# Kernel optimization log

Hardware: AMD Instinct MI355X
Metric: run time of the kernel (lower is better)

Reference implementation:

```python
import jax, jax.numpy as jnp
import numpy as np

D = 32        # dmodel (forced by reshape(..., 32) in the original)
N = 2000      # n_nodes == liner_fourth
SLOPE = 0.2   # LeakyReLU negative slope
EPS = 1e-6    # SublayerConnection LayerNorm eps (annotated-transformer style)


def _layernorm(x, g, b):
    m = x.mean(-1, keepdims=True)
    v = x.var(-1, keepdims=True)
    return g * (x - m) / jnp.sqrt(v + EPS) + b


def setup_inputs() -> dict:
    key = jax.random.key(0)
    ks = jax.random.split(key, 18)
    F_, NL, NS = 16, 500, 1500
    s = 0.1
    return {
        "state": jax.random.normal(ks[0], (F_, NS, D), jnp.float32),
        "left": jax.random.normal(ks[1], (F_, NL, D), jnp.float32),
        "inputad": jax.random.bernoulli(ks[2], 0.02, (F_, N, N)).astype(jnp.float32),
        "w3": s * jax.random.normal(ks[3], (D, D), jnp.float32),       # linearThird
        "b3": jnp.zeros((D,), jnp.float32),
        "attn_w": s * jax.random.normal(ks[4], (1, 2 * D), jnp.float32),  # attn (no bias)
        "w4": s * jax.random.normal(ks[5], (D, N), jnp.float32),       # linearFourth: 2000->32
        "b4": jnp.zeros((D,), jnp.float32),
        "w1": s * jax.random.normal(ks[6], (D, D), jnp.float32),       # linear
        "b1": jnp.zeros((D,), jnp.float32),
        "w_ih": s * jax.random.normal(ks[7], (4 * D, D), jnp.float32),  # LSTMCell (gate order i,f,g,o)
        "w_hh": s * jax.random.normal(ks[8], (4 * D, D), jnp.float32),
        "b_ih": jnp.zeros((4 * D,), jnp.float32),
        "b_hh": jnp.zeros((4 * D,), jnp.float32),
        "ln_g": jnp.ones((D,), jnp.float32),                            # SublayerConnection norm
        "ln_b": jnp.zeros((D,), jnp.float32),
        "w2": s * jax.random.normal(ks[9], (D, D), jnp.float32),        # linearSecond
        "b2": jnp.zeros((D,), jnp.float32),
    }


def reference(state, left, inputad, w3, b3, attn_w, w4, b4, w1, b1,
              w_ih, w_hh, b_ih, b_hh, ln_g, ln_b, w2, b2):
    # eval mode: all dropouts are identity
    x = jnp.concatenate([left, state], axis=1)          # [F, N, D]
    F_, n = x.shape[0], x.shape[1]
    g = x @ w3.T + b3                                   # [F, N, D]

    # torch: e = leaky(attn(cat([g.repeat_interleave(n,0), g.repeat(n,1,1)], -1)))
    # Decompose the linear over the concat: attn_w = [a_l | a_r].
    # g_repeat_interleave row m -> g[m // n]; g_repeat row m -> g[m % F_];
    # e.view(F_, n, n)[b, i, j] = e_flat[b*n + i, j].
    a_l, a_r = attn_w[0, :D], attn_w[0, D:]
    s_l = g @ a_l                                        # [F, N]
    s_r = g @ a_r                                        # [F, N]
    idx = (jnp.arange(F_)[:, None] * n + jnp.arange(n)[None, :]) % F_  # [F, N]
    e_mat = jax.nn.leaky_relu(s_l[:, None, :] + s_r[idx], SLOPE)       # [F, N, N]

    e_masked = jnp.where(inputad == 0, 0.0, e_mat)       # masked_fill(adj==0, 0)
    h = jax.nn.leaky_relu(jnp.einsum('bij,oj->bio', e_masked, w4) + b4, SLOPE)  # [F, N, 32]

    # first softmax(e)/dropout pair is dead code (overwritten); a = softmax(h, dim=1)
    a = jax.nn.softmax(h, axis=1)
    st = (a * g) @ w1.T + b1                             # elementwise branch (a.shape == g.shape)

    agg = jnp.matmul(inputad, st)                        # bmm(degree2, state): [F, N, D]

    # SublayerConnection: st + dropout(sublayer(norm(st))); sublayer = LSTMCell cell-state
    nx = _layernorm(st, ln_g, ln_b)
    c0 = nx.reshape(-1, D)                               # initial cell state = norm(st)
    # h0 = zeros, so the w_hh @ h0 contribution vanishes (b_hh still applies)
    gates = agg.reshape(-1, D) @ w_ih.T + b_ih + b_hh    # [F*N, 4D]
    i_g = jax.nn.sigmoid(gates[:, :D])
    f_g = jax.nn.sigmoid(gates[:, D:2 * D])
    g_g = jnp.tanh(gates[:, 2 * D:3 * D])
    c1 = f_g * c0 + i_g * g_g                            # LSTMCell returns (h', c'); [1] -> c'

    out = st + c1.reshape(F_, n, D)
    return out @ w2.T + b2
```

## Files before the change

### kernel.cpp

```cpp
#include <hip/hip_runtime.h>
#include <math.h>

#define F_    16
#define NROW  2000
#define NL    500
#define D     32
#define ROWS  (F_*NROW)
#define SLOPE 0.2f
#define CAP   128
#define LCAP  256

__global__ __launch_bounds__(256) void k1_g(
    const float* __restrict__ state, const float* __restrict__ left,
    const float* __restrict__ w3, const float* __restrict__ b3,
    const float* __restrict__ attn_w, const float* __restrict__ w4,
    float* __restrict__ g, float* __restrict__ s_l, float* __restrict__ s_r,
    float* __restrict__ w4t)
{
    int bid = blockIdx.x;
    int t = threadIdx.x;
    if (bid >= ROWS/8) {
        int k = (bid - ROWS/8) * 256 + t;
        if (k < D * NROW) {
            int o = k / NROW, j = k - o * NROW;
            w4t[j * D + o] = w4[k];
        }
        return;
    }
    __shared__ float sw3[D*33];
    __shared__ float sb3[D], sal[D], sar[D];
    for (int k = t; k < D*D; k += 256) sw3[(k>>5)*33 + (k&31)] = w3[k];
    if (t < D) { sb3[t] = b3[t]; sal[t] = attn_w[t]; sar[t] = attn_w[D + t]; }
    __syncthreads();
    int grp = t >> 5, lane = t & 31;
    int row = bid * 8 + grp;
    int b = row / NROW, i = row - b * NROW;
    const float* xrow = (i < NL) ? (left  + ((size_t)b * NL + i) * D)
                                 : (state + ((size_t)b * (NROW - NL) + (i - NL)) * D);
    float x = xrow[lane];
    float acc = sb3[lane];
#pragma unroll
    for (int k = 0; k < D; ++k)
        acc += __shfl(x, k, 32) * sw3[lane*33 + k];
    g[(size_t)row * D + lane] = acc;
    float pl = acc * sal[lane], pr = acc * sar[lane];
#pragma unroll
    for (int m = 16; m >= 1; m >>= 1) {
        pl += __shfl_xor(pl, m, 32);
        pr += __shfl_xor(pr, m, 32);
    }
    if (lane == 0) { s_l[row] = pl; s_r[row] = pr; }
}

__global__ __launch_bounds__(256) void k2_scan(
    const float* __restrict__ adj,
    const float* __restrict__ s_l, const float* __restrict__ s_r,
    const float* __restrict__ w4t, const float* __restrict__ b4,
    float* __restrict__ h, int* __restrict__ nzc, unsigned short* __restrict__ nzi)
{
    __shared__ int   sh_j[4][LCAP+1];
    __shared__ float sh_e[4][LCAP];
    int t = threadIdx.x;
    int w = t >> 6, lane = t & 63;
    int row = blockIdx.x * 4 + w;
    int b = row / NROW, i = row - b * NROW;
    int r = i & 15;
    const float4* mrow = reinterpret_cast<const float4*>(adj + (size_t)row * NROW);

    float4 v[8];
#pragma unroll
    for (int it = 0; it < 7; ++it)
        v[it] = mrow[it * 64 + lane];
    v[7] = make_float4(0.f, 0.f, 0.f, 0.f);
    if (448 + lane < NROW/4) v[7] = mrow[448 + lane];

    int c = 0;
#pragma unroll
    for (int it = 0; it < 8; ++it)
        c += (v[it].x != 0.f) + (v[it].y != 0.f) + (v[it].z != 0.f) + (v[it].w != 0.f);
    int inc = c;
#pragma unroll
    for (int off = 1; off < 64; off <<= 1) {
        int n = __shfl_up(inc, off, 64);
        inc += (lane >= off) ? n : 0;
    }
    int pos = inc - c;
    int cnt = __shfl(inc, 63, 64);

#pragma unroll
    for (int it = 0; it < 8; ++it) {
        int jb = (it * 64 + lane) * 4;
#pragma unroll
        for (int cc = 0; cc < 4; ++cc) {
            float val = (cc == 0) ? v[it].x : (cc == 1) ? v[it].y
                      : (cc == 2) ? v[it].z : v[it].w;
            int hit = (val != 0.f);
            int tgt = (hit && pos < LCAP) ? pos : LCAP;
            sh_j[w][tgt] = jb + cc;
            pos += hit;
        }
    }
    if (cnt > LCAP) cnt = LCAP;

    const float* slb = s_l + (size_t)b * NROW;
    const float* srr = s_r + (size_t)r * NROW;
    for (int k = lane; k < cnt; k += 64) {
        int j = sh_j[w][k];
        float e = slb[j] + srr[j];
        sh_e[w][k] = (e > 0.f) ? e : SLOPE * e;
    }

    int o = lane & 31, half = lane >> 5;
    float acc = 0.f;
    for (int k = half; k < cnt; k += 2)
        acc += sh_e[w][k] * w4t[sh_j[w][k] * D + o];
    acc += __shfl_xor(acc, 32, 64);
    if (lane < 32) {
        float hv = acc + b4[o];
        h[(size_t)row * D + o] = (hv > 0.f) ? hv : SLOPE * hv;
    }

    int cc2 = (cnt < CAP) ? cnt : CAP;
    for (int k = lane; k < cc2; k += 64)
        nzi[(size_t)row * CAP + k] = (unsigned short)sh_j[w][k];
    if (lane == 0) nzc[row] = cc2;
}

__global__ __launch_bounds__(256) void k3a_psum(const float* __restrict__ h,
                                                float* __restrict__ psum)
{
    int b = blockIdx.x, slice = blockIdx.y;
    int t = threadIdx.x;
    int o = t & 31, ti = t >> 5;
    int base = slice * 125;
    float s = 0.f;
    for (int i = base + ti; i < base + 125; i += 8)
        s += expf(h[((size_t)b * NROW + i) * D + o]);
    __shared__ float red[8][D];
    red[ti][o] = s;
    __syncthreads();
    if (t < D) {
        float tot = 0.f;
#pragma unroll
        for (int k = 0; k < 8; ++k) tot += red[k][t];
        psum[((size_t)b * 16 + slice) * D + t] = tot;
    }
}

__global__ __launch_bounds__(256) void k3b_st(
    const float* __restrict__ h, const float* __restrict__ g,
    const float* __restrict__ psum,
    const float* __restrict__ w1, const float* __restrict__ b1,
    float* __restrict__ st)
{
    __shared__ float sw1[D*33], sb1[D], ssum[D];
    int t = threadIdx.x;
    int bid = blockIdx.x;
    int b = bid / 250;
    for (int k = t; k < D*D; k += 256) sw1[(k>>5)*33 + (k&31)] = w1[k];
    if (t < D) {
        sb1[t] = b1[t];
        float tot = 0.f;
#pragma unroll
        for (int s = 0; s < 16; ++s) tot += psum[((size_t)b * 16 + s) * D + t];
        ssum[t] = tot;
    }
    __syncthreads();
    int grp = t >> 5, lane = t & 31;
    size_t row = (size_t)bid * 8 + grp;
    float p = (expf(h[row * D + lane]) / ssum[lane]) * g[row * D + lane];
    float acc = sb1[lane];
#pragma unroll
    for (int k = 0; k < D; ++k)
        acc += __shfl(p, k, 32) * sw1[lane*33 + k];
    st[row * D + lane] = acc;
}

__global__ __launch_bounds__(256) void k4_final(
    const float* __restrict__ st,
    const int* __restrict__ nzc, const unsigned short* __restrict__ nzi,
    const float* __restrict__ w_ih, const float* __restrict__ b_ih,
    const float* __restrict__ b_hh,
    const float* __restrict__ ln_g, const float* __restrict__ ln_b,
    const float* __restrict__ w2, const float* __restrict__ b2,
    float* __restrict__ out)
{
    __shared__ float swih[96*33];
    __shared__ float sw2[D*33];
    __shared__ float sbg[96];
    __shared__ float sb2[D], slg[D], slb[D];
    __shared__ unsigned short jl[8][CAP];
    __shared__ float aggsh[8][D];
    __shared__ float s2sh[8][D];

    int t = threadIdx.x;
    for (int k = t; k < 96*D; k += 256) swih[(k/D)*33 + (k%D)] = w_ih[k];
    for (int k = t; k < D*D;  k += 256) sw2 [(k/D)*33 + (k%D)] = w2[k];
    if (t < 96) sbg[t] = b_ih[t] + b_hh[t];
    if (t < D) { sb2[t] = b2[t]; slg[t] = ln_g[t]; slb[t] = ln_b[t]; }

    int grp = t >> 5, lane = t & 31;
    int row = blockIdx.x * 8 + grp;
    int b = row / NROW;
    int cnt = nzc[row];
    const unsigned short* lst = nzi + (size_t)row * CAP;
    for (int k = lane; k < cnt; k += 32) jl[grp][k] = lst[k];
    __syncthreads();

    const float* stb = st + (size_t)b * NROW * D;
    float agg = 0.f;
    int k = 0;
    for (; k + 8 <= cnt; k += 8) {
        int j0 = jl[grp][k],   j1 = jl[grp][k+1], j2 = jl[grp][k+2], j3 = jl[grp][k+3];
        int j4 = jl[grp][k+4], j5 = jl[grp][k+5], j6 = jl[grp][k+6], j7 = jl[grp][k+7];
        float a0 = stb[j0*D + lane], a1 = stb[j1*D + lane];
        float a2 = stb[j2*D + lane], a3 = stb[j3*D + lane];
        float a4 = stb[j4*D + lane], a5 = stb[j5*D + lane];
        float a6 = stb[j6*D + lane], a7 = stb[j7*D + lane];
        agg += ((a0 + a1) + (a2 + a3)) + ((a4 + a5) + (a6 + a7));
    }
    for (; k < cnt; ++k) agg += stb[jl[grp][k]*D + lane];

    float sv = st[(size_t)row * D + lane];

    float sum = sv;
#pragma unroll
    for (int m = 16; m >= 1; m >>= 1) sum += __shfl_xor(sum, m, 32);
    float mean = sum * (1.f / D);
    float dd = sv - mean;
    float vs = dd * dd;
#pragma unroll
    for (int m = 16; m >= 1; m >>= 1) vs += __shfl_xor(vs, m, 32);
    float inv = 1.f / sqrtf(vs * (1.f / D) + 1e-6f);
    float nx = slg[lane] * dd * inv + slb[lane];

    aggsh[grp][lane] = agg;

    float gi = sbg[lane], gf = sbg[lane + 32], gg = sbg[lane + 64];
#pragma unroll
    for (int d = 0; d < D; ++d) {
        float a = aggsh[grp][d];
        gi += swih[lane*33 + d]      * a;
        gf += swih[(lane+32)*33 + d] * a;
        gg += swih[(lane+64)*33 + d] * a;
    }
    float ig  = 1.f / (1.f + expf(-gi));
    float fg  = 1.f / (1.f + expf(-gf));
    float g_g = tanhf(gg);
    float s2  = sv + fg * nx + ig * g_g;

    s2sh[grp][lane] = s2;

    float acc = sb2[lane];
#pragma unroll
    for (int q = 0; q < D; ++q) acc += sw2[lane*33 + q] * s2sh[grp][q];
    out[(size_t)row * D + lane] = acc;
}

extern "C" void kernel_launch(void* const* d_in, const int* in_sizes, int n_in,
                              void* d_out, int out_size, void* d_ws, size_t ws_size,
                              hipStream_t stream)
{
    const float* state  = (const float*)d_in[0];
    const float* left   = (const float*)d_in[1];
    const float* adj    = (const float*)d_in[2];
    const float* w3     = (const float*)d_in[3];
    const float* b3     = (const float*)d_in[4];
    const float* attn_w = (const float*)d_in[5];
    const float* w4     = (const float*)d_in[6];
    const float* b4     = (const float*)d_in[7];
    const float* w1     = (const float*)d_in[8];
    const float* b1     = (const float*)d_in[9];
    const float* w_ih   = (const float*)d_in[10];
    const float* b_ih   = (const float*)d_in[12];
    const float* b_hh   = (const float*)d_in[13];
    const float* ln_g   = (const float*)d_in[14];
    const float* ln_b   = (const float*)d_in[15];
    const float* w2     = (const float*)d_in[16];
    const float* b2     = (const float*)d_in[17];
    float* out = (float*)d_out;

    float* g    = (float*)d_ws;
    float* h    = g  + (size_t)ROWS * D;
    float* st   = h  + (size_t)ROWS * D;
    float* s_l  = st + (size_t)ROWS * D;
    float* s_r  = s_l + ROWS;
    float* w4t  = s_r + ROWS;
    float* psum = w4t + (size_t)NROW * D;
    int*   nzc  = (int*)(psum + F_ * 16 * D);
    unsigned short* nzi = (unsigned short*)(nzc + ROWS);

    k1_g    <<<dim3(ROWS/8 + (D*NROW+255)/256), dim3(256), 0, stream>>>(
                state, left, w3, b3, attn_w, w4, g, s_l, s_r, w4t);
    k2_scan <<<dim3(ROWS/4),  dim3(256), 0, stream>>>(adj, s_l, s_r, w4t, b4, h, nzc, nzi);
    k3a_psum<<<dim3(F_, 16),  dim3(256), 0, stream>>>(h, psum);
    k3b_st  <<<dim3(ROWS/8),  dim3(256), 0, stream>>>(h, g, psum, w1, b1, st);
    k4_final<<<dim3(ROWS/8),  dim3(256), 0, stream>>>(st, nzc, nzi, w_ih, b_ih, b_hh,
                                                      ln_g, ln_b, w2, b2, out);
}
```

Before: 131.7 us.

## Split adjacency compaction from h gather into separate kernels with nontemporal loads

The fused scan kernel is split into two. The first streams the dense adjacency with nontemporal loads and writes only the compacted neighbour lists. The second uses 32-lane groups (8 rows per block) to compute the attention-weighted gather into h, unrolled by four so several w4t loads are in flight at once. The aim is to make the bandwidth-bound 256 MB adjacency read lean and decouple it from the latency-bound gather, at the cost of an extra launch and a round trip of nzi through global memory. The gather now also truncates to CAP (128) rather than LCAP (256) neighbours, which could change h for rows with more than 128 nonzeros.

```diff
diff --git a/kernel.cpp b/kernel.cpp
--- a/kernel.cpp
+++ b/kernel.cpp
@@ -9,6 +9,8 @@
 #define SLOPE 0.2f
 #define CAP   128
 #define LCAP  256
+
+typedef float f4 __attribute__((ext_vector_type(4)));
 
 __global__ __launch_bounds__(256) void k1_g(
     const float* __restrict__ state, const float* __restrict__ left,
@@ -52,32 +54,27 @@
     if (lane == 0) { s_l[row] = pl; s_r[row] = pr; }
 }
 
-__global__ __launch_bounds__(256) void k2_scan(
+__global__ __launch_bounds__(256) void k2a_compact(
     const float* __restrict__ adj,
-    const float* __restrict__ s_l, const float* __restrict__ s_r,
-    const float* __restrict__ w4t, const float* __restrict__ b4,
-    float* __restrict__ h, int* __restrict__ nzc, unsigned short* __restrict__ nzi)
-{
-    __shared__ int   sh_j[4][LCAP+1];
-    __shared__ float sh_e[4][LCAP];
+    int* __restrict__ nzc, unsigned short* __restrict__ nzi)
+{
+    __shared__ unsigned short sh_j[4][LCAP+8];
     int t = threadIdx.x;
     int w = t >> 6, lane = t & 63;
     int row = blockIdx.x * 4 + w;
-    int b = row / NROW, i = row - b * NROW;
-    int r = i & 15;
-    const float4* mrow = reinterpret_cast<const float4*>(adj + (size_t)row * NROW);
-
-    float4 v[8];
+    const f4* mrow = reinterpret_cast<const f4*>(adj + (size_t)row * NROW);
+
+    f4 v[8];
 #pragma unroll
     for (int it = 0; it < 7; ++it)
-        v[it] = mrow[it * 64 + lane];
-    v[7] = make_float4(0.f, 0.f, 0.f, 0.f);
-    if (448 + lane < NROW/4) v[7] = mrow[448 + lane];
+        v[it] = __builtin_nontemporal_load(mrow + it * 64 + lane);
+    v[7] = (f4)(0.f);
+    if (448 + lane < NROW/4) v[7] = __builtin_nontemporal_load(mrow + 448 + lane);
 
     int c = 0;
 #pragma unroll
     for (int it = 0; it < 8; ++it)
-        c += (v[it].x != 0.f) + (v[it].y != 0.f) + (v[it].z != 0.f) + (v[it].w != 0.f);
+        c += (v[it][0] != 0.f) + (v[it][1] != 0.f) + (v[it][2] != 0.f) + (v[it][3] != 0.f);
     int inc = c;
 #pragma unroll
     for (int off = 1; off < 64; off <<= 1) {
@@ -92,38 +89,56 @@
         int jb = (it * 64 + lane) * 4;
 #pragma unroll
         for (int cc = 0; cc < 4; ++cc) {
-            float val = (cc == 0) ? v[it].x : (cc == 1) ? v[it].y
-                      : (cc == 2) ? v[it].z : v[it].w;
+            float val = v[it][cc];
             int hit = (val != 0.f);
             int tgt = (hit && pos < LCAP) ? pos : LCAP;
-            sh_j[w][tgt] = jb + cc;
+            sh_j[w][tgt] = (unsigned short)(jb + cc);
             pos += hit;
         }
     }
-    if (cnt > LCAP) cnt = LCAP;
-
+    int cc2 = (cnt < CAP) ? cnt : CAP;
+    for (int k = lane; k < cc2; k += 64)
+        nzi[(size_t)row * CAP + k] = sh_j[w][k];
+    if (lane == 0) nzc[row] = cc2;
+}
+
+__global__ __launch_bounds__(256) void k2b_h(
+    const float* __restrict__ s_l, const float* __restrict__ s_r,
+    const float* __restrict__ w4t, const float* __restrict__ b4,
+    const int* __restrict__ nzc, const unsigned short* __restrict__ nzi,
+    float* __restrict__ h)
+{
+    __shared__ float sh_e[8][CAP];
+    __shared__ unsigned short sh_jj[8][CAP];
+    int t = threadIdx.x;
+    int grp = t >> 5, lane = t & 31;
+    int row = blockIdx.x * 8 + grp;
+    int b = row / NROW, i = row - b * NROW;
+    int r = i & 15;
+    int cnt = nzc[row];
+    const unsigned short* lst = nzi + (size_t)row * CAP;
     const float* slb = s_l + (size_t)b * NROW;
     const float* srr = s_r + (size_t)r * NROW;
-    for (int k = lane; k < cnt; k += 64) {
-        int j = sh_j[w][k];
+    for (int k = lane; k < cnt; k += 32) {
+        int j = lst[k];
+        sh_jj[grp][k] = (unsigned short)j;
         float e = slb[j] + srr[j];
-        sh_e[w][k] = (e > 0.f) ? e : SLOPE * e;
-    }
-
-    int o = lane & 31, half = lane >> 5;
+        sh_e[grp][k] = (e > 0.f) ? e : SLOPE * e;
+    }
     float acc = 0.f;
-    for (int k = half; k < cnt; k += 2)
-        acc += sh_e[w][k] * w4t[sh_j[w][k] * D + o];
-    acc += __shfl_xor(acc, 32, 64);
-    if (lane < 32) {
-        float hv = acc + b4[o];
-        h[(size_t)row * D + o] = (hv > 0.f) ? hv : SLOPE * hv;
-    }
-
-    int cc2 = (cnt < CAP) ? cnt : CAP;
-    for (int k = lane; k < cc2; k += 64)
-        nzi[(size_t)row * CAP + k] = (unsigned short)sh_j[w][k];
-    if (lane == 0) nzc[row] = cc2;
+    int k = 0;
+    for (; k + 4 <= cnt; k += 4) {
+        int j0 = sh_jj[grp][k],   j1 = sh_jj[grp][k+1];
+        int j2 = sh_jj[grp][k+2], j3 = sh_jj[grp][k+3];
+        float w0 = w4t[j0*D + lane], w1 = w4t[j1*D + lane];
+        float w2v = w4t[j2*D + lane], w3v = w4t[j3*D + lane];
+        acc += sh_e[grp][k]   * w0 + sh_e[grp][k+1] * w1
+             + sh_e[grp][k+2] * w2v + sh_e[grp][k+3] * w3v;
+    }
+    for (; k < cnt; ++k)
+        acc += sh_e[grp][k] * w4t[sh_jj[grp][k]*D + lane];
+    float hv = acc + b4[lane];
+    h[(size_t)row * D + lane] = (hv > 0.f) ? hv : SLOPE * hv;
 }
 
 __global__ __launch_bounds__(256) void k3a_psum(const float* __restrict__ h,
@@ -292,7 +307,8 @@
 
     k1_g    <<<dim3(ROWS/8 + (D*NROW+255)/256), dim3(256), 0, stream>>>(
                 state, left, w3, b3, attn_w, w4, g, s_l, s_r, w4t);
-    k2_scan <<<dim3(ROWS/4),  dim3(256), 0, stream>>>(adj, s_l, s_r, w4t, b4, h, nzc, nzi);
+    k2a_compact<<<dim3(ROWS/4), dim3(256), 0, stream>>>(adj, nzc, nzi);
+    k2b_h   <<<dim3(ROWS/8),  dim3(256), 0, stream>>>(s_l, s_r, w4t, b4, nzc, nzi, h);
     k3a_psum<<<dim3(F_, 16),  dim3(256), 0, stream>>>(h, psum);
     k3b_st  <<<dim3(ROWS/8),  dim3(256), 0, stream>>>(h, g, psum, w1, b1, st);
     k4_final<<<dim3(ROWS/8),  dim3(256), 0, stream>>>(st, nzc, nzi, w_ih, b_ih, b_hh,
```

New measurement: 132.8 us. Within noise of the previous version (+0.8%).
